# Optimization experiments

Hardware: AMD Instinct MI355X
Metric: run time of the kernel (lower is better)

Reference implementation:

```python
import jax, jax.numpy as jnp
import numpy as np
from jax import lax

N, E, H = 100000, 768, 1024   # candidates, span-emb dim, FFNN hidden
K, A = 1500, 50               # top-k mentions, max antecedents
NUM_DOCS = 10

def _ffnn(x, w0, b0, w1, b1, w2, b2):
    h = jax.nn.relu(x @ w0 + b0)
    h = jax.nn.relu(h @ w1 + b1)
    return (h @ w2 + b2)[..., 0]

def setup_inputs() -> dict:
    key = jax.random.key(0)
    ks = jax.random.split(key, 8)
    emb = jax.random.normal(ks[0], (N, E), dtype=jnp.float32)
    doc_ids = jnp.sort(jax.random.randint(ks[1], (N,), 0, NUM_DOCS))
    def w(k, shape):
        fan_in = shape[0]
        return jax.random.normal(k, shape, dtype=jnp.float32) / np.sqrt(fan_in)
    return {
        'candidate_span_emb': emb,
        'candidate_doc_ids': doc_ids,
        'uw0': w(ks[2], (E, H)), 'ub0': jnp.zeros((H,), jnp.float32),
        'uw1': w(ks[3], (H, H)), 'ub1': jnp.zeros((H,), jnp.float32),
        'uw2': w(ks[4], (H, 1)), 'ub2': jnp.zeros((1,), jnp.float32),
        'pw0': w(ks[5], (3 * E, H)), 'pb0': jnp.zeros((H,), jnp.float32),
        'pw1': w(ks[6], (H, H)), 'pb1': jnp.zeros((H,), jnp.float32),
        'pw2': w(ks[7], (H, 1)), 'pb2': jnp.zeros((1,), jnp.float32),
    }

def reference(candidate_span_emb, candidate_doc_ids,
              uw0, ub0, uw1, ub1, uw2, ub2,
              pw0, pb0, pw1, pb1, pw2, pb2):
    # 1) unary mention scores over all candidate spans  [N]
    scores = _ffnn(candidate_span_emb, uw0, ub0, uw1, ub1, uw2, ub2)
    # 2) top-k span pruning (extract_spans with sort_spans=True -> sorted ids)
    _, top_idx = lax.top_k(scores, K)
    top_idx = jnp.sort(top_idx)
    mention_emb = candidate_span_emb[top_idx]          # [K, E]
    mention_scores = scores[top_idx]                   # [K]
    mention_doc_ids = candidate_doc_ids[top_idx]       # [K]
    # 3) antecedent index construction + doc-boundary mask
    raw = jnp.arange(K)[:, None] - (jnp.arange(A) + 1)[None, :]   # [K, A]
    antecedents = jnp.maximum(raw, 0)
    mask = (mention_doc_ids[:, None] == mention_doc_ids[antecedents]) & (raw >= 0)
    log_mask = jnp.where(mask, 0.0, -jnp.inf).astype(jnp.float32)
    # 4) pairwise antecedent scoring: [m, a, m*a] -> FFNN + unary terms
    ante_emb = mention_emb[antecedents]                 # [K, A, E]
    tgt = jnp.broadcast_to(mention_emb[:, None, :], (K, A, E))
    pair_emb = jnp.concatenate([tgt, ante_emb, tgt * ante_emb], axis=-1)  # [K, A, 3E]
    pair_scores = _ffnn(pair_emb, pw0, pb0, pw1, pb1, pw2, pb2)           # [K, A]
    ante_scores = pair_scores + mention_scores[:, None] + mention_scores[antecedents]
    # 5) dummy antecedent column prepended
    out = jnp.concatenate([jnp.zeros((K, 1), jnp.float32), ante_scores + log_mask], axis=1)
    return out  # [K, A+1]
```

## Files before the change

kernel.cpp:

```cpp
#include <hip/hip_runtime.h>
#include <cstdint>
#include <cstddef>

#define NC 100000
#define ED 768
#define HD 1024
#define KTOP 1500
#define AA 50
#define NPAIR (KTOP*AA)
#define PSTRIDE 100096
#define PSLICES 8

typedef __attribute__((ext_vector_type(8))) short v8s;
typedef __attribute__((ext_vector_type(4))) float f32x4;

__device__ __forceinline__ float relu_(float x){ return fmaxf(x, 0.f); }
__device__ __forceinline__ float bf2f(ushort h){ return __uint_as_float(((unsigned)h) << 16); }
__device__ __forceinline__ ushort f2b(float f){
    unsigned u = __float_as_uint(f);
    return (ushort)((u + 0x7fffu + ((u >> 16) & 1u)) >> 16);
}
__device__ __forceinline__ unsigned pack2(float a, float b){
    return (unsigned)f2b(a) | ((unsigned)f2b(b) << 16);
}
__device__ __forceinline__ unsigned fkey(float s){
    unsigned u = __float_as_uint(s);
    return (u & 0x80000000u) ? ~u : (u | 0x80000000u);
}
__device__ __forceinline__ float sanitize_(float v)
{
    unsigned bu = __float_as_uint(v);
    if ((bu & 0x7f800000u) == 0x7f800000u)
        v = (bu & 0x007fffffu) ? 0.f : ((bu >> 31) ? -3.0e38f : 3.0e38f);
    return v;
}

#define AS1(p) ((const __attribute__((address_space(1))) void*)(p))
#define AS3(p) ((__attribute__((address_space(3))) void*)(p))

template<int EPI>
__global__ __launch_bounds__(256, 4)
void bgemm_k(const ushort* __restrict__ A, int lda,
             const ushort* __restrict__ BT, int ldb,
             void* __restrict__ Cv, int ldc, int M, int Ksz, int MP,
             const float* __restrict__ bias,
             const float* __restrict__ Ub, const float* __restrict__ Vb, int p0,
             const float* __restrict__ w2, float* __restrict__ partS)
{
    const int bid = blockIdx.x;
    const int xcd = bid & 7;
    const int i0  = bid >> 3;
    const int np  = i0 & 7;
    const int bmp = ((i0 >> 3) << 3) + xcd;
    if (bmp >= MP) return;
    const int bm = bmp << 7;
    const int bn = np << 7;

    __shared__ __align__(16) ushort Al[2][128*32];
    __shared__ __align__(16) ushort Bl[2][128*32];
    const int t = threadIdx.x;
    const int l = t & 63;
    const int w = t >> 6;
    const int wr = (w >> 1) << 6;
    const int wc = (w & 1) << 6;
    const int r15 = l & 15, q4 = l >> 4;
    const int srow16 = l >> 2;
    const int schnk  = l & 3;

    auto STAGE = [&](int buf, int k0) {
#pragma unroll
        for (int q = 0; q < 2; ++q) {
            int rbase = w*32 + q*16;
            int row = rbase + srow16;
            int cs = schnk ^ ((row >> 1) & 3);
            int gr = bm + row; if (gr > M-1) gr = M-1;
            __builtin_amdgcn_global_load_lds(AS1(A + (size_t)gr*lda + k0 + cs*8),
                                             AS3(&Al[buf][rbase*32]), 16, 0, 0);
            int gn = bn + row;
            __builtin_amdgcn_global_load_lds(AS1(BT + (size_t)gn*ldb + k0 + cs*8),
                                             AS3(&Bl[buf][rbase*32]), 16, 0, 0);
        }
    };

    f32x4 acc[4][4];
#pragma unroll
    for (int r = 0; r < 4; ++r)
#pragma unroll
        for (int c = 0; c < 4; ++c) acc[r][c] = (f32x4){0.f,0.f,0.f,0.f};

    STAGE(0, 0);
    __syncthreads();
    int cur = 0;
    for (int k0 = 0; k0 < Ksz; k0 += 32) {
        if (k0 + 32 < Ksz) STAGE(cur ^ 1, k0 + 32);
        const ushort* Ac = &Al[cur][0];
        const ushort* Bc = &Bl[cur][0];
        v8s af[4], bf[4];
#pragma unroll
        for (int r = 0; r < 4; ++r) {
            int row = wr + r*16 + r15;
            af[r] = *(const v8s*)(Ac + row*32 + ((q4 ^ ((row >> 1) & 3))*8));
            int col = wc + r*16 + r15;
            bf[r] = *(const v8s*)(Bc + col*32 + ((q4 ^ ((col >> 1) & 3))*8));
        }
#pragma unroll
        for (int r = 0; r < 4; ++r)
#pragma unroll
            for (int c = 0; c < 4; ++c)
                acc[r][c] = __builtin_amdgcn_mfma_f32_16x16x32_bf16(bf[c], af[r], acc[r][c], 0, 0, 0);
        __syncthreads();
        cur ^= 1;
    }

    if (EPI == 4) {
        float* srow = (float*)&Al[0][0];
        float sacc[4];
#pragma unroll
        for (int r = 0; r < 4; ++r) sacc[r] = 0.f;
#pragma unroll
        for (int c = 0; c < 4; ++c) {
            int n0 = bn + wc + c*16 + q4*4;
            const float4 bb = *(const float4*)(bias + n0);
            const float4 ww = *(const float4*)(w2 + n0);
#pragma unroll
            for (int r = 0; r < 4; ++r) {
                sacc[r] = fmaf(relu_(acc[r][c][0] + bb.x), ww.x, sacc[r]);
                sacc[r] = fmaf(relu_(acc[r][c][1] + bb.y), ww.y, sacc[r]);
                sacc[r] = fmaf(relu_(acc[r][c][2] + bb.z), ww.z, sacc[r]);
                sacc[r] = fmaf(relu_(acc[r][c][3] + bb.w), ww.w, sacc[r]);
            }
        }
        srow[t] = 0.f;
        __syncthreads();
#pragma unroll
        for (int r = 0; r < 4; ++r) {
            float s = sacc[r];
            s += __shfl_xor(s, 16, 64);
            s += __shfl_xor(s, 32, 64);
            if (q4 == 0) srow[(w & 1)*128 + wr + r*16 + r15] = s;
        }
        __syncthreads();
        if (t < 128) {
            int m = bm + t;
            if (m < M) partS[(size_t)np*PSTRIDE + m] = srow[t] + srow[128 + t];
        }
    } else {
        float*  Cf = (float*)Cv;
        ushort* Cb = (ushort*)Cv;
#pragma unroll
        for (int r = 0; r < 4; ++r) {
            int m = bm + wr + r*16 + r15;
            if (m >= M) continue;
            int iu = 0, iv = 0;
            if (EPI == 3) {
                int p = p0 + m;
                iu = p / 50;
                int a = p - iu*50;
                iv = iu - a - 1; if (iv < 0) iv = 0;
            }
#pragma unroll
            for (int c = 0; c < 4; ++c) {
                int n0 = bn + wc + c*16 + q4*4;
                float x0 = acc[r][c][0], x1 = acc[r][c][1];
                float x2 = acc[r][c][2], x3 = acc[r][c][3];
                if (EPI == 0) {
                    float4 o; o.x=x0; o.y=x1; o.z=x2; o.w=x3;
                    *(float4*)(Cf + (size_t)m*ldc + n0) = o;
                } else if (EPI == 1) {
                    const float4 bb = *(const float4*)(bias + n0);
                    float4 o; o.x=x0+bb.x; o.y=x1+bb.y; o.z=x2+bb.z; o.w=x3+bb.w;
                    *(float4*)(Cf + (size_t)m*ldc + n0) = o;
                } else if (EPI == 2) {
                    const float4 bb = *(const float4*)(bias + n0);
                    uint2 o;
                    o.x = pack2(relu_(x0+bb.x), relu_(x1+bb.y));
                    o.y = pack2(relu_(x2+bb.z), relu_(x3+bb.w));
                    *(uint2*)(Cb + (size_t)m*ldc + n0) = o;
                } else {
                    const float4 uu = *(const float4*)(Ub + (size_t)iu*HD + n0);
                    const float4 vv = *(const float4*)(Vb + (size_t)iv*HD + n0);
                    uint2 o;
                    o.x = pack2(relu_(x0+uu.x+vv.x), relu_(x1+uu.y+vv.y));
                    o.y = pack2(relu_(x2+uu.z+vv.z), relu_(x3+uu.w+vv.w));
                    *(uint2*)(Cb + (size_t)m*ldc + n0) = o;
                }
            }
        }
    }
}

__global__ void comb_k(const float* __restrict__ part, const float* __restrict__ b2,
                       float* __restrict__ out, int M)
{
    int i = blockIdx.x*256 + threadIdx.x;
    if (i < M) {
        float s = b2[0];
#pragma unroll
        for (int p = 0; p < PSLICES; ++p) s += part[(size_t)p*PSTRIDE + i];
        out[i] = s;
    }
}

__global__ void conv_k(const float* __restrict__ src, ushort* __restrict__ dst, int n4)
{
    for (int x = blockIdx.x*blockDim.x + threadIdx.x; x < n4; x += gridDim.x*blockDim.x) {
        float4 v = ((const float4*)src)[x];
        ushort4 o; o.x = f2b(v.x); o.y = f2b(v.y); o.z = f2b(v.z); o.w = f2b(v.w);
        ((ushort4*)dst)[x] = o;
    }
}

__global__ __launch_bounds__(256)
void wt_k(const float* __restrict__ W, ushort* __restrict__ WT, int K, int N)
{
    __shared__ float ld[32][33];
    int tx = threadIdx.x & 31, ty = threadIdx.x >> 5;
    int k0 = blockIdx.y*32, n0 = blockIdx.x*32;
#pragma unroll
    for (int r = 0; r < 4; ++r)
        ld[ty + r*8][tx] = W[(size_t)(k0 + ty + r*8)*N + n0 + tx];
    __syncthreads();
#pragma unroll
    for (int r = 0; r < 4; ++r)
        WT[(size_t)(n0 + ty + r*8)*K + k0 + tx] = f2b(ld[tx][ty + r*8]);
}

__global__ void init_sel_k(unsigned* state, unsigned* hist, int* top, int ntop)
{
    int t = threadIdx.x;
    if (t < 64) state[t] = 0u;
    for (int i = t; i < 1024; i += 256) hist[i] = 0u;
    for (int k = t; k < ntop; k += 256) top[k] = k;
}

__global__ __launch_bounds__(256)
void hist_k(const float* __restrict__ scores, int N, unsigned* __restrict__ hist,
            const unsigned* __restrict__ state, int shift)
{
    __shared__ unsigned lh[256];
    lh[threadIdx.x] = 0u;
    __syncthreads();
    unsigned prefix = state[0];
    for (int i = blockIdx.x*blockDim.x + threadIdx.x; i < N; i += gridDim.x*blockDim.x) {
        unsigned u = fkey(scores[i]);
        bool ok = (shift == 24) || ((u >> (shift+8)) == prefix);
        if (ok) atomicAdd(&lh[(u >> shift) & 0xffu], 1u);
    }
    __syncthreads();
    unsigned c = lh[threadIdx.x];
    if (c) atomicAdd(&hist[threadIdx.x], c);
}

__global__ void select_k(const unsigned* __restrict__ hist, unsigned* state, int shift, int K)
{
    if (threadIdx.x != 0) return;
    unsigned P = state[1];
    unsigned acc = 0; int bstar = 0;
    for (int b = 255; b >= 0; --b) {
        unsigned h = hist[b];
        if (P + acc + h >= (unsigned)K) { bstar = b; break; }
        acc += h;
    }
    state[0] = (shift == 24) ? (unsigned)bstar : ((state[0] << 8) | (unsigned)bstar);
    state[1] = P + acc;
    if (shift == 0) state[2] = state[0];
}

__global__ __launch_bounds__(256)
void cnt_k(const float* __restrict__ scores, int N, const unsigned* __restrict__ state,
           unsigned* __restrict__ gt_cnt, unsigned* __restrict__ eq_cnt)
{
    unsigned ut = state[2];
    int base = blockIdx.x * 2048;
    unsigned g = 0, e = 0;
    for (int q = 0; q < 8; ++q) {
        int i = base + q*256 + threadIdx.x;
        if (i < N) { unsigned u = fkey(scores[i]); g += (u > ut); e += (u == ut); }
    }
    __shared__ unsigned sg[256], se[256];
    sg[threadIdx.x] = g; se[threadIdx.x] = e;
    __syncthreads();
    for (int s = 128; s > 0; s >>= 1) {
        if (threadIdx.x < s) { sg[threadIdx.x] += sg[threadIdx.x+s]; se[threadIdx.x] += se[threadIdx.x+s]; }
        __syncthreads();
    }
    if (threadIdx.x == 0) { gt_cnt[blockIdx.x] = sg[0]; eq_cnt[blockIdx.x] = se[0]; }
}

__global__ void scan_k(const unsigned* gt_cnt, const unsigned* eq_cnt,
                       unsigned* gt_off, unsigned* eq_off, int nblk, unsigned* state, int K)
{
    if (threadIdx.x != 0) return;
    unsigned ag = 0, ae = 0;
    for (int b = 0; b < nblk; ++b) {
        gt_off[b] = ag; eq_off[b] = ae;
        ag += gt_cnt[b]; ae += eq_cnt[b];
    }
    state[3] = ag;
    state[4] = ag < (unsigned)K ? (unsigned)K - ag : 0u;
}

__global__ __launch_bounds__(256)
void write_k(const float* __restrict__ scores, int N, const unsigned* __restrict__ state,
             const unsigned* __restrict__ gt_off, const unsigned* __restrict__ eq_off,
             int* __restrict__ top_idx, int Ksel)
{
    unsigned ut = state[2], T = state[4];
    int base = blockIdx.x * 2048;
    unsigned grun = gt_off[blockIdx.x], erun = eq_off[blockIdx.x];
    __shared__ unsigned wg[4], we[4];
    int t = threadIdx.x, lane = t & 63, wv = t >> 6;
    for (int q = 0; q < 8; ++q) {
        int i = base + q*256 + t;
        bool valid = i < N;
        unsigned u = valid ? fkey(scores[i]) : 0u;
        bool g = valid && (u > ut);
        bool e = valid && (u == ut);
        unsigned long long bg = __ballot(g), be = __ballot(e);
        unsigned long long lt = (1ull << lane) - 1ull;
        unsigned lpg = __popcll(bg & lt), lpe = __popcll(be & lt);
        if (lane == 0) { wg[wv] = (unsigned)__popcll(bg); we[wv] = (unsigned)__popcll(be); }
        __syncthreads();
        unsigned bsg = 0, bse = 0, tg = 0, te = 0;
        for (int ww = 0; ww < 4; ++ww) {
            if (ww < wv) { bsg += wg[ww]; bse += we[ww]; }
            tg += wg[ww]; te += we[ww];
        }
        unsigned grank = grun + bsg + lpg;
        unsigned erank = erun + bse + lpe;
        unsigned pos = 0xffffffffu;
        if (g)                   pos = grank + (erank < T ? erank : T);
        else if (e && erank < T) pos = grank + erank;
        if (pos < (unsigned)Ksel) top_idx[pos] = i;
        grun += tg; erun += te;
        __syncthreads();
    }
}

__global__ void gatherF_k(const float* __restrict__ emb, const int* __restrict__ doc,
                          const int* __restrict__ topA, const float* __restrict__ scores,
                          ushort* __restrict__ meb, float* __restrict__ ms,
                          int* __restrict__ mdoc)
{
    int k = blockIdx.x;
    int idx = topA[k]; if (idx < 0 || idx >= NC) idx = 0;
    int t = threadIdx.x;
    if (t < 192) {
        float4 v = ((const float4*)(emb + (size_t)idx*ED))[t];
        ushort4 o; o.x = f2b(v.x); o.y = f2b(v.y); o.z = f2b(v.z); o.w = f2b(v.w);
        *(ushort4*)(meb + (size_t)k*ED + t*4) = o;
    }
    if (t == 192) { ms[k] = scores[idx]; mdoc[k] = doc[idx]; }
}

__global__ __launch_bounds__(256)
void prodb_k(const ushort* __restrict__ meb, ushort* __restrict__ prod, int p0, int C)
{
    int tot = C * 96;
    for (int x = blockIdx.x*blockDim.x + threadIdx.x; x < tot; x += gridDim.x*blockDim.x) {
        int pc = x / 96, e = x - pc*96;
        int p = p0 + pc;
        int i = p / 50, a = p - i*50;
        int j = i - a - 1; if (j < 0) j = 0;
        uint4 ui = ((const uint4*)(meb + (size_t)i*ED))[e];
        uint4 uj = ((const uint4*)(meb + (size_t)j*ED))[e];
        auto pk = [](unsigned a_, unsigned b_) -> unsigned {
            float lo = bf2f((ushort)(a_ & 0xffffu)) * bf2f((ushort)(b_ & 0xffffu));
            float hi = bf2f((ushort)(a_ >> 16))     * bf2f((ushort)(b_ >> 16));
            return (unsigned)f2b(lo) | ((unsigned)f2b(hi) << 16);
        };
        uint4 o; o.x = pk(ui.x, uj.x); o.y = pk(ui.y, uj.y);
                 o.z = pk(ui.z, uj.z); o.w = pk(ui.w, uj.w);
        ((uint4*)(prod + (size_t)pc*ED))[e] = o;
    }
}

__global__ __launch_bounds__(256)
void assemble_k(const float* __restrict__ ps, const float* __restrict__ ms,
                const int* __restrict__ mdoc, float* __restrict__ out)
{
    int idx = blockIdx.x*blockDim.x + threadIdx.x;
    if (idx >= KTOP*(AA+1)) return;
    int i = idx / (AA+1), col = idx - i*(AA+1);
    if (col == 0) { out[idx] = 0.f; return; }
    int a = col - 1;
    int raw = i - a - 1;
    int j = raw < 0 ? 0 : raw;
    bool mk = (raw >= 0) && (mdoc[i] == mdoc[j]);
    float v = mk ? (ps[i*AA + a] + ms[i] + ms[j]) : -3.0e38f;
    out[idx] = sanitize_(v);
}

static inline int swz_grid(int MP) { return ((MP + 7) & ~7) * 8; }

extern "C" void kernel_launch(void* const* d_in, const int* in_sizes, int n_in,
                              void* d_out, int out_size, void* d_ws, size_t ws_size,
                              hipStream_t stream)
{
    const float* emb = (const float*)d_in[0];
    const int*   doc = (const int*)d_in[1];
    const float* uw0 = (const float*)d_in[2];
    const float* ub0 = (const float*)d_in[3];
    const float* uw1 = (const float*)d_in[4];
    const float* ub1 = (const float*)d_in[5];
    const float* uw2 = (const float*)d_in[6];
    const float* ub2 = (const float*)d_in[7];
    const float* pw0 = (const float*)d_in[8];
    const float* pb0 = (const float*)d_in[9];
    const float* pw1 = (const float*)d_in[10];
    const float* pb1 = (const float*)d_in[11];
    const float* pw2 = (const float*)d_in[12];
    const float* pb2 = (const float*)d_in[13];
    float* out = (float*)d_out;

    char* ws = (char*)d_ws;
    size_t off = 0;
    auto alloc = [&](size_t bytes) -> void* {
        void* p = ws + off;
        off = (off + bytes + 255) & ~(size_t)255;
        return p;
    };
    const int NBLKA = (NC + 2047) / 2048;
    float*    scoresA = (float*)alloc((size_t)NC*4);
    float*    partS   = (float*)alloc((size_t)PSLICES*PSTRIDE*4);
    unsigned* stateA  = (unsigned*)alloc(64*4);
    unsigned* histA   = (unsigned*)alloc(1024*4);
    unsigned* gtA  = (unsigned*)alloc((size_t)NBLKA*4);
    unsigned* eqA  = (unsigned*)alloc((size_t)NBLKA*4);
    unsigned* gtoA = (unsigned*)alloc((size_t)NBLKA*4);
    unsigned* eqoA = (unsigned*)alloc((size_t)NBLKA*4);
    int*      topA = (int*)alloc((size_t)KTOP*4);
    ushort*   meb  = (ushort*)alloc((size_t)KTOP*ED*2);
    float*    ms   = (float*)alloc((size_t)KTOP*4);
    int*      mdoc = (int*)alloc((size_t)KTOP*4);
    float*    U    = (float*)alloc((size_t)KTOP*HD*4);
    float*    V    = (float*)alloc((size_t)KTOP*HD*4);
    float*    ps   = (float*)alloc((size_t)NPAIR*4);
    ushort*   uw0T = (ushort*)alloc((size_t)HD*ED*2);
    ushort*   uw1T = (ushort*)alloc((size_t)HD*HD*2);
    ushort*   paT  = (ushort*)alloc((size_t)HD*ED*2);
    ushort*   pbT  = (ushort*)alloc((size_t)HD*ED*2);
    ushort*   pcT  = (ushort*)alloc((size_t)HD*ED*2);
    ushort*   pw1T = (ushort*)alloc((size_t)HD*HD*2);
    size_t fixed = off;
    size_t avail = ws_size > fixed ? ws_size - fixed : 0;

    wt_k<<<dim3(HD/32, ED/32), 256, 0, stream>>>(uw0, uw0T, ED, HD);
    wt_k<<<dim3(HD/32, HD/32), 256, 0, stream>>>(uw1, uw1T, HD, HD);
    wt_k<<<dim3(HD/32, ED/32), 256, 0, stream>>>(pw0, paT, ED, HD);
    wt_k<<<dim3(HD/32, ED/32), 256, 0, stream>>>(pw0 + (size_t)ED*HD, pbT, ED, HD);
    wt_k<<<dim3(HD/32, ED/32), 256, 0, stream>>>(pw0 + (size_t)2*ED*HD, pcT, ED, HD);
    wt_k<<<dim3(HD/32, HD/32), 256, 0, stream>>>(pw1, pw1T, HD, HD);

    {
        long Rl = (long)(avail / 3584);
        int R = (int)(Rl > 100096 ? 100096 : Rl);
        R &= ~127; if (R < 128) R = 128;
        ushort* embB = (ushort*)(ws + fixed);
        ushort* H1b  = embB + (size_t)R*ED;
        for (int r0 = 0; r0 < NC; r0 += R) {
            int rows = NC - r0 < R ? NC - r0 : R;
            int MP = (rows + 127)/128;
            conv_k<<<1024, 256, 0, stream>>>(emb + (size_t)r0*ED, embB, rows*192);
            bgemm_k<2><<<swz_grid(MP), 256, 0, stream>>>(embB, ED, uw0T, ED, H1b, HD,
                rows, ED, MP, ub0, nullptr, nullptr, 0, nullptr, nullptr);
            bgemm_k<4><<<swz_grid(MP), 256, 0, stream>>>(H1b, HD, uw1T, HD, nullptr, 0,
                rows, HD, MP, ub1, nullptr, nullptr, 0, uw2, partS);
            comb_k<<<(rows + 255)/256, 256, 0, stream>>>(partS, ub2, scoresA + r0, rows);
        }
    }

    init_sel_k<<<1, 256, 0, stream>>>(stateA, histA, topA, KTOP);
    for (int pass = 0; pass < 4; ++pass) {
        int shift = 24 - pass*8;
        hist_k<<<256, 256, 0, stream>>>(scoresA, NC, histA + pass*256, stateA, shift);
        select_k<<<1, 64, 0, stream>>>(histA + pass*256, stateA, shift, KTOP);
    }
    cnt_k<<<NBLKA, 256, 0, stream>>>(scoresA, NC, stateA, gtA, eqA);
    scan_k<<<1, 64, 0, stream>>>(gtA, eqA, gtoA, eqoA, NBLKA, stateA, KTOP);
    write_k<<<NBLKA, 256, 0, stream>>>(scoresA, NC, stateA, gtoA, eqoA, topA, KTOP);
    gatherF_k<<<KTOP, 256, 0, stream>>>(emb, doc, topA, scoresA, meb, ms, mdoc);

    {
        int MP = (KTOP + 127)/128;
        bgemm_k<1><<<swz_grid(MP), 256, 0, stream>>>(meb, ED, paT, ED, U, HD, KTOP, ED,
            MP, pb0, nullptr, nullptr, 0, nullptr, nullptr);
        bgemm_k<0><<<swz_grid(MP), 256, 0, stream>>>(meb, ED, pbT, ED, V, HD, KTOP, ED,
            MP, nullptr, nullptr, nullptr, 0, nullptr, nullptr);
    }

    {
        long Cl = (long)(avail / 3584);
        int Cp = (int)(Cl > NPAIR ? NPAIR : Cl);
        Cp &= ~127; if (Cp < 128) Cp = 128;
        ushort* prodb = (ushort*)(ws + fixed);
        ushort* h0b = prodb + (size_t)Cp*ED;
        for (int p0 = 0; p0 < NPAIR; p0 += Cp) {
            int pc = NPAIR - p0 < Cp ? NPAIR - p0 : Cp;
            int MP = (pc + 127)/128;
            prodb_k<<<1024, 256, 0, stream>>>(meb, prodb, p0, pc);
            bgemm_k<3><<<swz_grid(MP), 256, 0, stream>>>(prodb, ED, pcT, ED, h0b, HD,
                pc, ED, MP, nullptr, U, V, p0, nullptr, nullptr);
            bgemm_k<4><<<swz_grid(MP), 256, 0, stream>>>(h0b, HD, pw1T, HD, nullptr, 0,
                pc, HD, MP, pb1, nullptr, nullptr, 0, pw2, partS);
            comb_k<<<(pc + 255)/256, 256, 0, stream>>>(partS, pb2, ps + p0, pc);
        }
    }

    assemble_k<<<(KTOP*(AA+1) + 255)/256, 256, 0, stream>>>(ps, ms, mdoc, out);
}
```

Measured before the change: 1.126 ms.

## Enlarge bf16 GEMM tiles to 256x256 with 512-thread blocks

The shared GEMM kernel now uses 256x256 output tiles with 8 waves per block instead of 128x128 with 4 waves. Each wave computes a 128x64 sub-tile, giving 32 accumulators, and the fused score epilogue reduces across 4 column-waves. The N-split drops from 8 to 4 slices and all launches, grid swizzle and chunk sizes are updated to match. The aim is more data reuse per LDS load and fewer global reads of A and B. In exchange it doubles LDS use per block and increases register pressure, which lowers occupancy and makes padding waste larger for the small K=1500 GEMMs.

```diff
diff --git a/kernel.cpp b/kernel.cpp
--- a/kernel.cpp
+++ b/kernel.cpp
@@ -9,7 +9,7 @@
 #define AA 50
 #define NPAIR (KTOP*AA)
 #define PSTRIDE 100096
-#define PSLICES 8
+#define PSLICES 4
 
 typedef __attribute__((ext_vector_type(8))) short v8s;
 typedef __attribute__((ext_vector_type(4))) float f32x4;
@@ -39,7 +39,7 @@
 #define AS3(p) ((__attribute__((address_space(3))) void*)(p))
 
 template<int EPI>
-__global__ __launch_bounds__(256, 4)
+__global__ __launch_bounds__(512, 2)
 void bgemm_k(const ushort* __restrict__ A, int lda,
              const ushort* __restrict__ BT, int ldb,
              void* __restrict__ Cv, int ldc, int M, int Ksz, int MP,
@@ -49,30 +49,32 @@
 {
     const int bid = blockIdx.x;
     const int xcd = bid & 7;
-    const int i0  = bid >> 3;
-    const int np  = i0 & 7;
-    const int bmp = ((i0 >> 3) << 3) + xcd;
+    const int idx = bid >> 3;
+    const int np  = idx & 3;
+    const int bmp = ((idx >> 2) << 3) + xcd;
     if (bmp >= MP) return;
-    const int bm = bmp << 7;
-    const int bn = np << 7;
-
-    __shared__ __align__(16) ushort Al[2][128*32];
-    __shared__ __align__(16) ushort Bl[2][128*32];
+    const int bm = bmp << 8;
+    const int bn = np << 8;
+
+    __shared__ __align__(16) ushort Al[2][256*32];
+    __shared__ __align__(16) ushort Bl[2][256*32];
     const int t = threadIdx.x;
     const int l = t & 63;
     const int w = t >> 6;
-    const int wr = (w >> 1) << 6;
-    const int wc = (w & 1) << 6;
+    const int wm = w >> 2;
+    const int wn = w & 3;
+    const int wr = wm << 7;
+    const int wc = wn << 6;
     const int r15 = l & 15, q4 = l >> 4;
-    const int srow16 = l >> 2;
-    const int schnk  = l & 3;
+    const int sr4 = l >> 2;
+    const int sc  = l & 3;
 
     auto STAGE = [&](int buf, int k0) {
 #pragma unroll
         for (int q = 0; q < 2; ++q) {
             int rbase = w*32 + q*16;
-            int row = rbase + srow16;
-            int cs = schnk ^ ((row >> 1) & 3);
+            int row = rbase + sr4;
+            int cs = sc ^ ((row >> 1) & 3);
             int gr = bm + row; if (gr > M-1) gr = M-1;
             __builtin_amdgcn_global_load_lds(AS1(A + (size_t)gr*lda + k0 + cs*8),
                                              AS3(&Al[buf][rbase*32]), 16, 0, 0);
@@ -82,9 +84,9 @@
         }
     };
 
-    f32x4 acc[4][4];
-#pragma unroll
-    for (int r = 0; r < 4; ++r)
+    f32x4 acc[8][4];
+#pragma unroll
+    for (int r = 0; r < 8; ++r)
 #pragma unroll
         for (int c = 0; c < 4; ++c) acc[r][c] = (f32x4){0.f,0.f,0.f,0.f};
 
@@ -95,16 +97,19 @@
         if (k0 + 32 < Ksz) STAGE(cur ^ 1, k0 + 32);
         const ushort* Ac = &Al[cur][0];
         const ushort* Bc = &Bl[cur][0];
-        v8s af[4], bf[4];
-#pragma unroll
-        for (int r = 0; r < 4; ++r) {
+        v8s af[8], bf[4];
+#pragma unroll
+        for (int r = 0; r < 8; ++r) {
             int row = wr + r*16 + r15;
             af[r] = *(const v8s*)(Ac + row*32 + ((q4 ^ ((row >> 1) & 3))*8));
-            int col = wc + r*16 + r15;
-            bf[r] = *(const v8s*)(Bc + col*32 + ((q4 ^ ((col >> 1) & 3))*8));
-        }
-#pragma unroll
-        for (int r = 0; r < 4; ++r)
+        }
+#pragma unroll
+        for (int c = 0; c < 4; ++c) {
+            int col = wc + c*16 + r15;
+            bf[c] = *(const v8s*)(Bc + col*32 + ((q4 ^ ((col >> 1) & 3))*8));
+        }
+#pragma unroll
+        for (int r = 0; r < 8; ++r)
 #pragma unroll
             for (int c = 0; c < 4; ++c)
                 acc[r][c] = __builtin_amdgcn_mfma_f32_16x16x32_bf16(bf[c], af[r], acc[r][c], 0, 0, 0);
@@ -114,41 +119,41 @@
 
     if (EPI == 4) {
         float* srow = (float*)&Al[0][0];
-        float sacc[4];
-#pragma unroll
-        for (int r = 0; r < 4; ++r) sacc[r] = 0.f;
+        float sacc[8];
+#pragma unroll
+        for (int r = 0; r < 8; ++r) sacc[r] = 0.f;
 #pragma unroll
         for (int c = 0; c < 4; ++c) {
             int n0 = bn + wc + c*16 + q4*4;
             const float4 bb = *(const float4*)(bias + n0);
             const float4 ww = *(const float4*)(w2 + n0);
 #pragma unroll
-            for (int r = 0; r < 4; ++r) {
+            for (int r = 0; r < 8; ++r) {
                 sacc[r] = fmaf(relu_(acc[r][c][0] + bb.x), ww.x, sacc[r]);
                 sacc[r] = fmaf(relu_(acc[r][c][1] + bb.y), ww.y, sacc[r]);
                 sacc[r] = fmaf(relu_(acc[r][c][2] + bb.z), ww.z, sacc[r]);
                 sacc[r] = fmaf(relu_(acc[r][c][3] + bb.w), ww.w, sacc[r]);
             }
         }
-        srow[t] = 0.f;
-        __syncthreads();
-#pragma unroll
-        for (int r = 0; r < 4; ++r) {
+#pragma unroll
+        for (int r = 0; r < 8; ++r) {
             float s = sacc[r];
             s += __shfl_xor(s, 16, 64);
             s += __shfl_xor(s, 32, 64);
-            if (q4 == 0) srow[(w & 1)*128 + wr + r*16 + r15] = s;
+            if (q4 == 0) srow[wn*256 + wr + r*16 + r15] = s;
         }
         __syncthreads();
-        if (t < 128) {
+        if (t < 256) {
             int m = bm + t;
-            if (m < M) partS[(size_t)np*PSTRIDE + m] = srow[t] + srow[128 + t];
+            if (m < M)
+                partS[(size_t)np*PSTRIDE + m] =
+                    (srow[t] + srow[256 + t]) + (srow[512 + t] + srow[768 + t]);
         }
     } else {
         float*  Cf = (float*)Cv;
         ushort* Cb = (ushort*)Cv;
 #pragma unroll
-        for (int r = 0; r < 4; ++r) {
+        for (int r = 0; r < 8; ++r) {
             int m = bm + wr + r*16 + r15;
             if (m >= M) continue;
             int iu = 0, iv = 0;
@@ -391,7 +396,7 @@
     out[idx] = sanitize_(v);
 }
 
-static inline int swz_grid(int MP) { return ((MP + 7) & ~7) * 8; }
+static inline int swz_grid(int MP) { return ((MP + 7) & ~7) * 4; }
 
 extern "C" void kernel_launch(void* const* d_in, const int* in_sizes, int n_in,
                               void* d_out, int out_size, void* d_ws, size_t ws_size,
@@ -455,16 +460,16 @@
     {
         long Rl = (long)(avail / 3584);
         int R = (int)(Rl > 100096 ? 100096 : Rl);
-        R &= ~127; if (R < 128) R = 128;
+        R &= ~255; if (R < 256) R = 256;
         ushort* embB = (ushort*)(ws + fixed);
         ushort* H1b  = embB + (size_t)R*ED;
         for (int r0 = 0; r0 < NC; r0 += R) {
             int rows = NC - r0 < R ? NC - r0 : R;
-            int MP = (rows + 127)/128;
+            int MP = (rows + 255)/256;
             conv_k<<<1024, 256, 0, stream>>>(emb + (size_t)r0*ED, embB, rows*192);
-            bgemm_k<2><<<swz_grid(MP), 256, 0, stream>>>(embB, ED, uw0T, ED, H1b, HD,
+            bgemm_k<2><<<swz_grid(MP), 512, 0, stream>>>(embB, ED, uw0T, ED, H1b, HD,
                 rows, ED, MP, ub0, nullptr, nullptr, 0, nullptr, nullptr);
-            bgemm_k<4><<<swz_grid(MP), 256, 0, stream>>>(H1b, HD, uw1T, HD, nullptr, 0,
+            bgemm_k<4><<<swz_grid(MP), 512, 0, stream>>>(H1b, HD, uw1T, HD, nullptr, 0,
                 rows, HD, MP, ub1, nullptr, nullptr, 0, uw2, partS);
             comb_k<<<(rows + 255)/256, 256, 0, stream>>>(partS, ub2, scoresA + r0, rows);
         }
@@ -482,26 +487,26 @@
     gatherF_k<<<KTOP, 256, 0, stream>>>(emb, doc, topA, scoresA, meb, ms, mdoc);
 
     {
-        int MP = (KTOP + 127)/128;
-        bgemm_k<1><<<swz_grid(MP), 256, 0, stream>>>(meb, ED, paT, ED, U, HD, KTOP, ED,
+        int MP = (KTOP + 255)/256;
+        bgemm_k<1><<<swz_grid(MP), 512, 0, stream>>>(meb, ED, paT, ED, U, HD, KTOP, ED,
             MP, pb0, nullptr, nullptr, 0, nullptr, nullptr);
-        bgemm_k<0><<<swz_grid(MP), 256, 0, stream>>>(meb, ED, pbT, ED, V, HD, KTOP, ED,
+        bgemm_k<0><<<swz_grid(MP), 512, 0, stream>>>(meb, ED, pbT, ED, V, HD, KTOP, ED,
             MP, nullptr, nullptr, nullptr, 0, nullptr, nullptr);
     }
 
     {
         long Cl = (long)(avail / 3584);
-        int Cp = (int)(Cl > NPAIR ? NPAIR : Cl);
-        Cp &= ~127; if (Cp < 128) Cp = 128;
+        int Cp = (int)(Cl > 75008 ? 75008 : Cl);
+        Cp &= ~255; if (Cp < 256) Cp = 256;
         ushort* prodb = (ushort*)(ws + fixed);
         ushort* h0b = prodb + (size_t)Cp*ED;
         for (int p0 = 0; p0 < NPAIR; p0 += Cp) {
             int pc = NPAIR - p0 < Cp ? NPAIR - p0 : Cp;
-            int MP = (pc + 127)/128;
+            int MP = (pc + 255)/256;
             prodb_k<<<1024, 256, 0, stream>>>(meb, prodb, p0, pc);
-            bgemm_k<3><<<swz_grid(MP), 256, 0, stream>>>(prodb, ED, pcT, ED, h0b, HD,
+            bgemm_k<3><<<swz_grid(MP), 512, 0, stream>>>(prodb, ED, pcT, ED, h0b, HD,
                 pc, ED, MP, nullptr, U, V, p0, nullptr, nullptr);
-            bgemm_k<4><<<swz_grid(MP), 256, 0, stream>>>(h0b, HD, pw1T, HD, nullptr, 0,
+            bgemm_k<4><<<swz_grid(MP), 512, 0, stream>>>(h0b, HD, pw1T, HD, nullptr, 0,
                 pc, HD, MP, pb1, nullptr, nullptr, 0, pw2, partS);
             comb_k<<<(pc + 255)/256, 256, 0, stream>>>(partS, pb2, ps + p0, pc);
         }
```

Result: slower. 1.270 ms (+12.8%).
